# Optimization experiments

Hardware: AMD Instinct MI355X
Metric: run time of the kernel (lower is better)

Reference implementation:

```python
import jax, jax.numpy as jnp
import numpy as np

N_NODES = 50000
N_EDGES = 600000
D_IN = 128
D_OUT = 128


def setup_inputs() -> dict:
    key = jax.random.key(0)
    ks = jax.random.split(key, 6)
    gain = float(np.sqrt(2.0))  # relu gain for xavier init
    lim = gain * np.sqrt(6.0 / (D_IN + D_IN))
    pool_w = jax.random.uniform(ks[0], (D_IN, D_IN), jnp.float32, -lim, lim)
    lim2 = gain * np.sqrt(6.0 / (D_IN + D_OUT))
    lin_w = jax.random.uniform(ks[1], (D_OUT, D_IN), jnp.float32, -lim2, lim2)
    return {
        "node_feats": jax.random.normal(ks[2], (N_NODES, D_IN), jnp.float32),
        "src": jax.random.randint(ks[3], (N_EDGES,), 0, N_NODES, jnp.int32),
        "dst": jax.random.randint(ks[4], (N_EDGES,), 0, N_NODES, jnp.int32),
        "e_weight": jax.random.uniform(ks[5], (N_EDGES,), jnp.float32),
        "pool_w": pool_w,
        "pool_b": jnp.zeros((D_IN,), jnp.float32),
        "lin_w": lin_w,
        "lin_b": jnp.zeros((D_OUT,), jnp.float32),
        "bias": jnp.zeros((D_OUT,), jnp.float32),
    }


def reference(node_feats, src, dst, e_weight, pool_w, pool_b, lin_w, lin_b, bias):
    # maxpool aggregator: h_src = relu(pool(x) + pool_bias)   [N, D_IN]
    h_src = jax.nn.relu(node_feats @ pool_w.T + pool_b)
    # u_mul_e message: gather src features, scale by edge weight  [E, D_IN]
    m = h_src[src] * e_weight[:, None]
    # fn.max reduce per destination node; empty mailboxes -> 0
    h_new = jax.ops.segment_max(m, dst, num_segments=N_NODES)
    h_new = jnp.where(jnp.isfinite(h_new), h_new, 0.0)
    # final linear (+its bias) + extra bias parameter
    return h_new @ lin_w.T + lin_b + bias
```

## Files before the change

### kernel.cpp

```cpp
#include <hip/hip_runtime.h>
#include <hip/hip_bf16.h>

#define NN 50000
#define NE 600000
#define DD 128
#define CAP 48

typedef __attribute__((ext_vector_type(8))) short short8_t;
typedef __attribute__((ext_vector_type(4))) short short4_t;
typedef __attribute__((ext_vector_type(4))) float f32x4;

__device__ __forceinline__ short f2bf(float f) {
    union { float f; unsigned u; } v; v.f = f;
    unsigned r = (v.u + 0x7FFFu + ((v.u >> 16) & 1u)) >> 16;
    return (short)r;
}
__device__ __forceinline__ unsigned pk2(float lo, float hi) {
    __hip_bfloat162 h(__float2bfloat16(lo), __float2bfloat16(hi));
    unsigned u; __builtin_memcpy(&u, &h, 4); return u;
}
__device__ __forceinline__ float bflo(unsigned x) { return __uint_as_float(x << 16); }
__device__ __forceinline__ float bfhi(unsigned x) { return __uint_as_float(x & 0xffff0000u); }

__device__ __forceinline__ void gl16(const void* g, void* l) {
    __builtin_amdgcn_global_load_lds(
        (const __attribute__((address_space(1))) unsigned*)g,
        (__attribute__((address_space(3))) unsigned*)l, 16, 0, 0);
}

__global__ __launch_bounds__(512) void gemm1(const float* __restrict__ A,
        const float* __restrict__ Wp, const float* __restrict__ b1,
        unsigned short* __restrict__ hout, const float* __restrict__ Wl,
        unsigned short* __restrict__ wimg)
{
    __shared__ short aL[128 * 128];
    __shared__ short wL[128 * 128];
    const int tid = threadIdx.x;
    const int m0 = blockIdx.x * 128;

    if (blockIdx.x == 0) {
        #pragma unroll
        for (int i = 0; i < 8; ++i) {
            int idx = (i * 512 + tid) * 4;
            int row = idx >> 7;
            int kk = (idx & 127) ^ ((row & 7) << 3);
            float4 v = *(const float4*)(Wl + row * 128 + kk);
            uint2 o = { pk2(v.x, v.y), pk2(v.z, v.w) };
            *(uint2*)(wimg + idx) = o;
        }
    }

    #pragma unroll
    for (int i = 0; i < 8; ++i) {
        int flat = i * 2048 + tid * 4;
        int row = flat >> 7, k = flat & 127;
        int gr = m0 + row;
        float4 v = make_float4(0.f, 0.f, 0.f, 0.f);
        if (gr < NN) v = *(const float4*)(A + (size_t)gr * 128 + k);
        uint2 o = { pk2(v.x, v.y), pk2(v.z, v.w) };
        *(uint2*)(aL + ((row * 128 + k) ^ ((row & 7) << 3))) = o;
    }
    #pragma unroll
    for (int i = 0; i < 8; ++i) {
        int flat = i * 2048 + tid * 4;
        int row = flat >> 7, k = flat & 127;
        float4 v = *(const float4*)(Wp + flat);
        uint2 o = { pk2(v.x, v.y), pk2(v.z, v.w) };
        *(uint2*)(wL + ((row * 128 + k) ^ ((row & 7) << 3))) = o;
    }
    __syncthreads();

    const int lane = tid & 63, wid = tid >> 6;
    const int l15 = lane & 15, lhi = lane >> 4;
    const int r0 = wid * 16;
    f32x4 acc[8];
    #pragma unroll
    for (int t = 0; t < 8; ++t) acc[t] = f32x4{0.f, 0.f, 0.f, 0.f};

    #pragma unroll
    for (int kk = 0; kk < 4; ++kk) {
        const int k0 = kk * 32 + lhi * 8;
        const int ar = r0 + l15;
        short8_t a = *(short8_t*)(aL + ((ar * 128 + k0) ^ ((ar & 7) << 3)));
        #pragma unroll
        for (int t = 0; t < 8; ++t) {
            const int br = t * 16 + l15;
            short8_t b = *(short8_t*)(wL + ((br * 128 + k0) ^ ((br & 7) << 3)));
            acc[t] = __builtin_amdgcn_mfma_f32_16x16x32_bf16(a, b, acc[t], 0, 0, 0);
        }
    }

    #pragma unroll
    for (int t = 0; t < 8; ++t) {
        const int c = t * 16 + l15;
        float add = b1[c];
        #pragma unroll
        for (int i = 0; i < 4; ++i) {
            int r = m0 + r0 + lhi * 4 + i;
            if (r < NN) {
                float v = fmaxf(acc[t][i] + add, 0.f);
                hout[(size_t)r * 128 + (c ^ ((r & 7) << 3))] = (unsigned short)f2bf(v);
            }
        }
    }
}

#define BT 150000
__global__ __launch_bounds__(256) void bucket(const int* __restrict__ src,
        const int* __restrict__ dst, const float* __restrict__ ew,
        int* __restrict__ counts, unsigned* __restrict__ edges)
{
    const int t = blockIdx.x * 256 + threadIdx.x;
    if (t >= BT) return;
    int d[4], s[4]; float w[4];
    #pragma unroll
    for (int u = 0; u < 4; ++u) {
        const int e = t + u * BT;
        d[u] = dst[e]; s[u] = src[e]; w[u] = ew[e];
    }
    int pos[4];
    #pragma unroll
    for (int u = 0; u < 4; ++u)
        pos[u] = atomicAdd(&counts[d[u] << 4], 1);
    #pragma unroll
    for (int u = 0; u < 4; ++u)
        if (pos[u] < CAP)
            edges[(size_t)d[u] * CAP + pos[u]] =
                ((unsigned)s[u] << 16) | (unsigned short)f2bf(w[u]);
}

template<int NIT>
__device__ __forceinline__ void gat(const unsigned short* __restrict__ hb,
        unsigned p, int deg, int g, int l16, float* m)
{
    #pragma unroll
    for (int it = 0; it < NIT; ++it) {
        const int ia = it * 8 + g, ib = it * 8 + 4 + g;
        unsigned pa = __shfl(p, ia), pb = __shfl(p, ib);
        float wa = (ia < deg) ? __uint_as_float(pa << 16) : 0.f;
        float wb = (ib < deg) ? __uint_as_float(pb << 16) : 0.f;
        unsigned sa = pa >> 16, sb = pb >> 16;
        uint4 ra = *(const uint4*)(hb + (size_t)sa * 128 + ((l16 * 8) ^ ((sa & 7) << 3)));
        uint4 rb = *(const uint4*)(hb + (size_t)sb * 128 + ((l16 * 8) ^ ((sb & 7) << 3)));
        m[0] = fmaxf(m[0], bflo(ra.x) * wa); m[1] = fmaxf(m[1], bfhi(ra.x) * wa);
        m[2] = fmaxf(m[2], bflo(ra.y) * wa); m[3] = fmaxf(m[3], bfhi(ra.y) * wa);
        m[4] = fmaxf(m[4], bflo(ra.z) * wa); m[5] = fmaxf(m[5], bfhi(ra.z) * wa);
        m[6] = fmaxf(m[6], bflo(ra.w) * wa); m[7] = fmaxf(m[7], bfhi(ra.w) * wa);
        m[0] = fmaxf(m[0], bflo(rb.x) * wb); m[1] = fmaxf(m[1], bfhi(rb.x) * wb);
        m[2] = fmaxf(m[2], bflo(rb.y) * wb); m[3] = fmaxf(m[3], bfhi(rb.y) * wb);
        m[4] = fmaxf(m[4], bflo(rb.z) * wb); m[5] = fmaxf(m[5], bfhi(rb.z) * wb);
        m[6] = fmaxf(m[6], bflo(rb.w) * wb); m[7] = fmaxf(m[7], bfhi(rb.w) * wb);
    }
}

#define NMB 2048
__global__ __launch_bounds__(256) void node_max(const unsigned short* __restrict__ hb,
        const int* __restrict__ counts, const unsigned* __restrict__ edges,
        unsigned short* __restrict__ hnew)
{
    const int lane = threadIdx.x & 63;
    const int g = lane >> 4, l16 = lane & 15;
    for (int base = blockIdx.x * 4 + (threadIdx.x >> 6); base < NN; base += NMB * 4) {
        const int node = base;
        const int deg = min(counts[node << 4], CAP);
        const unsigned* ep = edges + (size_t)node * CAP;
        unsigned p = (lane < deg) ? ep[lane] : 0u;

        float m[8];
        #pragma unroll
        for (int i = 0; i < 8; ++i) m[i] = 0.f;

        if (deg <= 16)      gat<2>(hb, p, deg, g, l16, m);
        else if (deg <= 32) gat<4>(hb, p, deg, g, l16, m);
        else                gat<6>(hb, p, deg, g, l16, m);

        #pragma unroll
        for (int i = 0; i < 8; ++i) {
            m[i] = fmaxf(m[i], __shfl_xor(m[i], 16));
            m[i] = fmaxf(m[i], __shfl_xor(m[i], 32));
        }

        if (g == 0) {
            uint4 o;
            o.x = pk2(m[0], m[1]);
            o.y = pk2(m[2], m[3]);
            o.z = pk2(m[4], m[5]);
            o.w = pk2(m[6], m[7]);
            *(uint4*)(hnew + (size_t)node * 128 + ((l16 * 8) ^ ((node & 7) << 3))) = o;
        }
    }
}

__global__ __launch_bounds__(512) void gemm2(const unsigned short* __restrict__ Aimg,
        const unsigned short* __restrict__ wimg, const float* __restrict__ b1,
        const float* __restrict__ b2, float* __restrict__ out)
{
    __shared__ short aL[128 * 128];
    __shared__ short wL[128 * 128];
    const int tid = threadIdx.x;
    const int lane = tid & 63, wid = tid >> 6;
    const int m0 = blockIdx.x * 128;

    #pragma unroll
    for (int i = 0; i < 4; ++i) {
        const int soff = i * 4096 + wid * 512;
        gl16(Aimg + (size_t)m0 * 128 + soff + lane * 8, aL + soff);
        gl16(wimg + soff + lane * 8, wL + soff);
    }
    __syncthreads();

    const int l15 = lane & 15, lhi = lane >> 4;
    const int r0 = wid * 16;
    f32x4 acc[8];
    #pragma unroll
    for (int t = 0; t < 8; ++t) acc[t] = f32x4{0.f, 0.f, 0.f, 0.f};

    #pragma unroll
    for (int kk = 0; kk < 4; ++kk) {
        const int k0 = kk * 32 + lhi * 8;
        const int ar = r0 + l15;
        short8_t a = *(short8_t*)(aL + ((ar * 128 + k0) ^ ((ar & 7) << 3)));
        #pragma unroll
        for (int t = 0; t < 8; ++t) {
            const int br = t * 16 + l15;
            short8_t b = *(short8_t*)(wL + ((br * 128 + k0) ^ ((br & 7) << 3)));
            acc[t] = __builtin_amdgcn_mfma_f32_16x16x32_bf16(a, b, acc[t], 0, 0, 0);
        }
    }

    #pragma unroll
    for (int t = 0; t < 8; ++t) {
        const int c = t * 16 + l15;
        float add = b1[c] + b2[c];
        #pragma unroll
        for (int i = 0; i < 4; ++i) {
            int r = m0 + r0 + lhi * 4 + i;
            if (r < NN) out[(size_t)r * 128 + c] = acc[t][i] + add;
        }
    }
}

extern "C" void kernel_launch(void* const* d_in, const int* in_sizes, int n_in,
                              void* d_out, int out_size, void* d_ws, size_t ws_size,
                              hipStream_t stream) {
    const float* node_feats = (const float*)d_in[0];
    const int*   src        = (const int*)d_in[1];
    const int*   dst        = (const int*)d_in[2];
    const float* ew         = (const float*)d_in[3];
    const float* pool_w     = (const float*)d_in[4];
    const float* pool_b     = (const float*)d_in[5];
    const float* lin_w      = (const float*)d_in[6];
    const float* lin_b      = (const float*)d_in[7];
    const float* bias       = (const float*)d_in[8];
    float* out = (float*)d_out;

    char* w0 = (char*)d_ws;
    unsigned short* hsrc = (unsigned short*)w0;  w0 += (size_t)NN * DD * 2;
    unsigned short* hnew = (unsigned short*)w0;  w0 += (size_t)NN * DD * 2;
    int* counts = (int*)w0;                      w0 += (size_t)NN * 64;
    unsigned* edges = (unsigned*)w0;             w0 += (size_t)NN * CAP * 4;
    unsigned short* wimg = (unsigned short*)w0;  w0 += (size_t)DD * DD * 2;

    hipMemsetAsync(counts, 0, (size_t)NN * 64, stream);

    const int gemm_grid = (NN + 127) / 128;
    gemm1<<<gemm_grid, 512, 0, stream>>>(node_feats, pool_w, pool_b, hsrc,
                                         lin_w, wimg);

    bucket<<<(BT + 255) / 256, 256, 0, stream>>>(src, dst, ew, counts, edges);

    node_max<<<NMB, 256, 0, stream>>>(hsrc, counts, edges, hnew);

    gemm2<<<gemm_grid, 512, 0, stream>>>(hnew, wimg, lin_b, bias, out);
}
```

Baseline: 169.7 us.

## Fuse edge bucketing into first GEMM launch and halve GEMM row tile

Merges the bucket kernel into the first GEMM kernel as extra blocks, so one launch handles both and the independent work can run concurrently. The GEMM row tile drops from 128 to 64 rows per block, with waves split across two 64-column halves and A fragments hoisted into registers; LDS use falls and launch bounds request higher occupancy. The cost is that each block reloads the full weight tile for half as many rows, and bucket blocks now share the launch with the heavier GEMM blocks.

```diff
diff --git a/kernel.cpp b/kernel.cpp
--- a/kernel.cpp
+++ b/kernel.cpp
@@ -5,9 +5,11 @@
 #define NE 600000
 #define DD 128
 #define CAP 48
+#define BT 150000
+#define BUCKB 293
+#define GEMMB 782
 
 typedef __attribute__((ext_vector_type(8))) short short8_t;
-typedef __attribute__((ext_vector_type(4))) short short4_t;
 typedef __attribute__((ext_vector_type(4))) float f32x4;
 
 __device__ __forceinline__ short f2bf(float f) {
@@ -28,17 +30,43 @@
         (__attribute__((address_space(3))) unsigned*)l, 16, 0, 0);
 }
 
-__global__ __launch_bounds__(512) void gemm1(const float* __restrict__ A,
+__global__ __launch_bounds__(512, 6) void fused1(const float* __restrict__ A,
         const float* __restrict__ Wp, const float* __restrict__ b1,
         unsigned short* __restrict__ hout, const float* __restrict__ Wl,
-        unsigned short* __restrict__ wimg)
-{
-    __shared__ short aL[128 * 128];
+        unsigned short* __restrict__ wimg, int* __restrict__ counts,
+        const int* __restrict__ src, const int* __restrict__ dst,
+        const float* __restrict__ ew, unsigned* __restrict__ edges)
+{
+    __shared__ short aL[64 * 128];
     __shared__ short wL[128 * 128];
     const int tid = threadIdx.x;
-    const int m0 = blockIdx.x * 128;
-
-    if (blockIdx.x == 0) {
+
+    if (blockIdx.x < BUCKB) {
+        const int t = blockIdx.x * 512 + tid;
+        if (t < BT) {
+            int d[4], s[4]; float w[4];
+            #pragma unroll
+            for (int u = 0; u < 4; ++u) {
+                const int e = t + u * BT;
+                d[u] = dst[e]; s[u] = src[e]; w[u] = ew[e];
+            }
+            int pos[4];
+            #pragma unroll
+            for (int u = 0; u < 4; ++u)
+                pos[u] = atomicAdd(&counts[d[u] << 4], 1);
+            #pragma unroll
+            for (int u = 0; u < 4; ++u)
+                if (pos[u] < CAP)
+                    edges[(size_t)d[u] * CAP + pos[u]] =
+                        ((unsigned)s[u] << 16) | (unsigned short)f2bf(w[u]);
+        }
+        return;
+    }
+
+    const int gb = blockIdx.x - BUCKB;
+    const int m0 = gb * 64;
+
+    if (gb == 0) {
         #pragma unroll
         for (int i = 0; i < 8; ++i) {
             int idx = (i * 512 + tid) * 4;
@@ -51,7 +79,7 @@
     }
 
     #pragma unroll
-    for (int i = 0; i < 8; ++i) {
+    for (int i = 0; i < 4; ++i) {
         int flat = i * 2048 + tid * 4;
         int row = flat >> 7, k = flat & 127;
         int gr = m0 + row;
@@ -72,27 +100,33 @@
 
     const int lane = tid & 63, wid = tid >> 6;
     const int l15 = lane & 15, lhi = lane >> 4;
-    const int r0 = wid * 16;
-    f32x4 acc[8];
-    #pragma unroll
-    for (int t = 0; t < 8; ++t) acc[t] = f32x4{0.f, 0.f, 0.f, 0.f};
-
+    const int rg = wid & 3, cs = wid >> 2;
+    const int r0 = rg * 16;
+
+    short8_t af[4];
     #pragma unroll
     for (int kk = 0; kk < 4; ++kk) {
-        const int k0 = kk * 32 + lhi * 8;
         const int ar = r0 + l15;
-        short8_t a = *(short8_t*)(aL + ((ar * 128 + k0) ^ ((ar & 7) << 3)));
-        #pragma unroll
-        for (int t = 0; t < 8; ++t) {
-            const int br = t * 16 + l15;
-            short8_t b = *(short8_t*)(wL + ((br * 128 + k0) ^ ((br & 7) << 3)));
-            acc[t] = __builtin_amdgcn_mfma_f32_16x16x32_bf16(a, b, acc[t], 0, 0, 0);
-        }
-    }
-
-    #pragma unroll
-    for (int t = 0; t < 8; ++t) {
-        const int c = t * 16 + l15;
+        af[kk] = *(short8_t*)(aL + ((ar * 128 + kk * 32 + lhi * 8) ^ ((ar & 7) << 3)));
+    }
+
+    f32x4 acc[4];
+    #pragma unroll
+    for (int t = 0; t < 4; ++t) acc[t] = f32x4{0.f, 0.f, 0.f, 0.f};
+
+    #pragma unroll
+    for (int t = 0; t < 4; ++t) {
+        const int br = cs * 64 + t * 16 + l15;
+        #pragma unroll
+        for (int kk = 0; kk < 4; ++kk) {
+            short8_t b = *(short8_t*)(wL + ((br * 128 + kk * 32 + lhi * 8) ^ ((br & 7) << 3)));
+            acc[t] = __builtin_amdgcn_mfma_f32_16x16x32_bf16(af[kk], b, acc[t], 0, 0, 0);
+        }
+    }
+
+    #pragma unroll
+    for (int t = 0; t < 4; ++t) {
+        const int c = cs * 64 + t * 16 + l15;
         float add = b1[c];
         #pragma unroll
         for (int i = 0; i < 4; ++i) {
@@ -103,30 +137,6 @@
             }
         }
     }
-}
-
-#define BT 150000
-__global__ __launch_bounds__(256) void bucket(const int* __restrict__ src,
-        const int* __restrict__ dst, const float* __restrict__ ew,
-        int* __restrict__ counts, unsigned* __restrict__ edges)
-{
-    const int t = blockIdx.x * 256 + threadIdx.x;
-    if (t >= BT) return;
-    int d[4], s[4]; float w[4];
-    #pragma unroll
-    for (int u = 0; u < 4; ++u) {
-        const int e = t + u * BT;
-        d[u] = dst[e]; s[u] = src[e]; w[u] = ew[e];
-    }
-    int pos[4];
-    #pragma unroll
-    for (int u = 0; u < 4; ++u)
-        pos[u] = atomicAdd(&counts[d[u] << 4], 1);
-    #pragma unroll
-    for (int u = 0; u < 4; ++u)
-        if (pos[u] < CAP)
-            edges[(size_t)d[u] * CAP + pos[u]] =
-                ((unsigned)s[u] << 16) | (unsigned short)f2bf(w[u]);
 }
 
 template<int NIT>
@@ -160,8 +170,7 @@
 {
     const int lane = threadIdx.x & 63;
     const int g = lane >> 4, l16 = lane & 15;
-    for (int base = blockIdx.x * 4 + (threadIdx.x >> 6); base < NN; base += NMB * 4) {
-        const int node = base;
+    for (int node = blockIdx.x * 4 + (threadIdx.x >> 6); node < NN; node += NMB * 4) {
         const int deg = min(counts[node << 4], CAP);
         const unsigned* ep = edges + (size_t)node * CAP;
         unsigned p = (lane < deg) ? ep[lane] : 0u;
@@ -263,13 +272,10 @@
 
     hipMemsetAsync(counts, 0, (size_t)NN * 64, stream);
 
-    const int gemm_grid = (NN + 127) / 128;
-    gemm1<<<gemm_grid, 512, 0, stream>>>(node_feats, pool_w, pool_b, hsrc,
-                                         lin_w, wimg);
-
-    bucket<<<(BT + 255) / 256, 256, 0, stream>>>(src, dst, ew, counts, edges);
+    fused1<<<BUCKB + GEMMB, 512, 0, stream>>>(node_feats, pool_w, pool_b, hsrc,
+            lin_w, wimg, counts, src, dst, ew, edges);
 
     node_max<<<NMB, 256, 0, stream>>>(hsrc, counts, edges, hnew);
 
-    gemm2<<<gemm_grid, 512, 0, stream>>>(hnew, wimg, lin_b, bias, out);
-}
+    gemm2<<<(NN + 127) / 128, 512, 0, stream>>>(hnew, wimg, lin_b, bias, out);
+}
```

Result: faster. 164.7 us (-2.9%).
